# Kernel tuning notes

Hardware: AMD Instinct MI355X
Metric: run time of the kernel (lower is better)

Reference implementation:

```python
import jax, jax.numpy as jnp
import numpy as np

K_SIM_SCHEDULE = [4, 8, 16]
K_CON_SCHEDULE = [2, 4, 8]
NEG = 1000000000.0


def _dual_adjacency(h, k_sim, k_con):
    """Binary causal dual adjacency (similar / dissimilar), no gradient."""
    B, T, D = h.shape
    h = jax.lax.stop_gradient(h)
    xn = h / jnp.maximum(jnp.linalg.norm(h, axis=-1, keepdims=True), 1e-12)
    sim = jnp.einsum('btd,bsd->bts', xn, xn)                 # (B,T,T)
    past = jnp.tril(jnp.ones((T, T), h.dtype), -1)           # strictly-past mask
    sim = sim * past - NEG * (1.0 - past)
    eff_sim = min(k_sim, T - 1)
    eff_con = min(k_con, max(0, T - 1 - eff_sim))
    bI = jnp.arange(B)[:, None, None]
    tI = jnp.arange(T)[None, :, None]
    A_sim = jnp.zeros((B, T, T), h.dtype)
    if eff_sim > 0:
        _, top_idx = jax.lax.top_k(sim, eff_sim)             # (B,T,k)
        A_sim = A_sim.at[bI, tI, top_idx].set(1.0) * past
    A_con = jnp.zeros((B, T, T), h.dtype)
    if eff_con > 0:
        sim_con = jnp.where(A_sim > 0, NEG, sim)
        _, bot_idx = jax.lax.top_k(-sim_con, eff_con)        # smallest eff_con
        A_con = A_con.at[bI, tI, bot_idx].set(1.0) * past * (1.0 - A_sim)
    return A_sim, A_con


def _aggregate(h, A):
    # unweighted mean over selected neighbors; empty rows -> zeros
    deg = jnp.sum(A, axis=-1, keepdims=True)
    return jnp.einsum('bts,bsd->btd', A, h) / jnp.maximum(deg, 1.0)


def setup_inputs() -> dict:
    key = jax.random.key(0)
    ks = jax.random.split(key, 2)
    B, T, D, R = 4, 2048, 512, 3
    x = jax.random.normal(ks[0], (B, T, D), dtype=jnp.float32)
    gain = jnp.ones((R, D), dtype=jnp.float32)
    bias = jnp.zeros((R, D), dtype=jnp.float32)
    log_mix = jnp.zeros((R,), dtype=jnp.float32)
    log_alpha = jnp.zeros((R,), dtype=jnp.float32)
    log_momentum = jnp.asarray(1.0, dtype=jnp.float32)
    log_scale = jnp.asarray(0.0, dtype=jnp.float32)
    return {"x": x, "gain": gain, "bias": bias, "log_mix": log_mix,
            "log_alpha": log_alpha, "log_momentum": log_momentum,
            "log_scale": log_scale}


def reference(x, gain, bias, log_mix, log_alpha, log_momentum, log_scale):
    momentum = jax.nn.sigmoid(log_momentum)
    scale = jax.nn.softplus(log_scale) + 0.01
    h = x
    for r in range(len(K_SIM_SCHEDULE)):
        mix = jax.nn.sigmoid(log_mix[r])
        alpha = jax.nn.sigmoid(log_alpha[r])
        A_sim, A_con = _dual_adjacency(h, K_SIM_SCHEDULE[r], K_CON_SCHEDULE[r])
        msg_pos = _aggregate(h, A_sim)
        msg_neg = _aggregate(h, A_con)
        ctx = alpha * msg_pos + (1.0 - alpha) * msg_neg
        blended = mix * h + (1.0 - mix) * ctx
        h_new = jax.nn.gelu(blended * gain[r] + bias[r], approximate=False)
        h = momentum * h + (1.0 - momentum) * h_new
    return (h - x) * scale
```

## Files before the change

kernel.cpp:

```cpp
#include <hip/hip_runtime.h>
#include <hip/hip_bf16.h>
#include <cstdint>
#include <cstddef>

#define BB 4
#define TT 2048
#define DD 512
#define NEG_INF (-3.402823466e+38f)
#define POS_INF (3.402823466e+38f)

typedef __attribute__((ext_vector_type(8))) short bf16x8;
typedef __attribute__((ext_vector_type(8))) unsigned short ushort8;
typedef __attribute__((ext_vector_type(4))) float f32x4;

__device__ __forceinline__ float sigmoidf_(float x){ return 1.0f/(1.0f+expf(-x)); }

__device__ __forceinline__ unsigned short f2bf(float x){
  __hip_bfloat16 b = __float2bfloat16(x);
  return *reinterpret_cast<unsigned short*>(&b);
}

__device__ __forceinline__ unsigned int fwd_map(float f){
  unsigned int b = __float_as_uint(f);
  return b ^ ((b & 0x80000000u) ? 0xFFFFFFFFu : 0x80000000u);
}
__device__ __forceinline__ float inv_map(unsigned int u){
  unsigned int b = (u & 0x80000000u) ? (u ^ 0x80000000u) : ~u;
  return __uint_as_float(b);
}

__global__ __launch_bounds__(64) void k_normsplit(const float* __restrict__ h, float* __restrict__ rnorm,
                                                  unsigned short* __restrict__ Xh, unsigned short* __restrict__ Xl){
  int row = blockIdx.x;
  const float* hr = h + (size_t)row*DD;
  int lane = threadIdx.x;
  float4 v0 = *(const float4*)&hr[lane*4];
  float4 v1 = *(const float4*)&hr[lane*4 + 256];
  float ss = v0.x*v0.x+v0.y*v0.y+v0.z*v0.z+v0.w*v0.w
           + v1.x*v1.x+v1.y*v1.y+v1.z*v1.z+v1.w*v1.w;
  #pragma unroll
  for (int off=32; off; off>>=1) ss += __shfl_xor(ss, off);
  float rn = 1.0f / fmaxf(sqrtf(ss), 1e-12f);
  if (lane==0) rnorm[row] = rn;

  float xs[8] = {v0.x,v0.y,v0.z,v0.w,v1.x,v1.y,v1.z,v1.w};
  unsigned short hb[8], lb[8];
  #pragma unroll
  for (int q=0;q<8;q++){
    float xn = xs[q]*rn;
    unsigned short hh = f2bf(xn);
    __hip_bfloat16 bh = *reinterpret_cast<__hip_bfloat16*>(&hh);
    float rem = xn - __bfloat162float(bh);
    hb[q] = hh; lb[q] = f2bf(rem);
  }
  ushort4 h0 = {hb[0],hb[1],hb[2],hb[3]}, h1 = {hb[4],hb[5],hb[6],hb[7]};
  ushort4 l0 = {lb[0],lb[1],lb[2],lb[3]}, l1 = {lb[4],lb[5],lb[6],lb[7]};
  *(ushort4*)&Xh[(size_t)row*DD + lane*4]       = h0;
  *(ushort4*)&Xh[(size_t)row*DD + lane*4 + 256] = h1;
  *(ushort4*)&Xl[(size_t)row*DD + lane*4]       = l0;
  *(ushort4*)&Xl[(size_t)row*DD + lane*4 + 256] = l1;
}

__global__ __launch_bounds__(256) void k_sim(const unsigned short* __restrict__ Xh,
                                             const unsigned short* __restrict__ Xl,
                                             float* __restrict__ sim, int b0){
  int p = blockIdx.x;
  int jt = (int)((sqrtf(8.0f*(float)p + 1.0f) - 1.0f)*0.5f);
  while ((jt+1)*(jt+2)/2 <= p) jt++;
  while (jt*(jt+1)/2 > p) jt--;
  int is = p - jt*(jt+1)/2;

  int bl = blockIdx.y;
  size_t xoff = (size_t)(b0 + bl)*TT*DD;
  const unsigned short* XhB = Xh + xoff;
  const unsigned short* XlB = Xl + xoff;
  float* simb = sim + (size_t)bl*TT*TT;
  int t0 = jt*128, s0 = is*128;

  __shared__ __align__(16) short As[128*32];
  __shared__ __align__(16) short Bs[128*32];

  int tid = threadIdx.x, wave = tid>>6, lane = tid&63;
  int wr = wave>>1, wc = wave&1;

  int srow = tid>>2;
  int sc8  = (tid&3)*8;

  f32x4 acc[4][4];
  #pragma unroll
  for (int m=0;m<4;m++)
    #pragma unroll
    for (int n=0;n<4;n++) acc[m][n] = (f32x4){0.f,0.f,0.f,0.f};

  ushort8 ra0, ra1, rb0, rb1;
  auto gload = [&](int s){
    int pass = s>>4; int kcol = (s&15)*32;
    const unsigned short* sA = (pass<2) ? XhB : XlB;
    const unsigned short* sB = (pass!=1) ? XhB : XlB;
    ra0 = *(const ushort8*)&sA[(size_t)(t0+srow)*DD + kcol + sc8];
    ra1 = *(const ushort8*)&sA[(size_t)(t0+srow+64)*DD + kcol + sc8];
    rb0 = *(const ushort8*)&sB[(size_t)(s0+srow)*DD + kcol + sc8];
    rb1 = *(const ushort8*)&sB[(size_t)(s0+srow+64)*DD + kcol + sc8];
  };

  gload(0);
  for (int s=0; s<48; ++s){
    __syncthreads();
    *(ushort8*)&As[srow*32 + sc8]      = ra0;
    *(ushort8*)&As[(srow+64)*32 + sc8] = ra1;
    *(ushort8*)&Bs[srow*32 + sc8]      = rb0;
    *(ushort8*)&Bs[(srow+64)*32 + sc8] = rb1;
    __syncthreads();
    if (s < 47) gload(s+1);

    int arow = wr*64 + (lane&15);
    int brow = wc*64 + (lane&15);
    int kb = (lane>>4)*8;
    bf16x8 af[4], bf[4];
    #pragma unroll
    for (int m=0;m<4;m++) af[m] = *(const bf16x8*)&As[(arow + m*16)*32 + kb];
    #pragma unroll
    for (int n=0;n<4;n++) bf[n] = *(const bf16x8*)&Bs[(brow + n*16)*32 + kb];
    #pragma unroll
    for (int m=0;m<4;m++)
      #pragma unroll
      for (int n=0;n<4;n++)
        acc[m][n] = __builtin_amdgcn_mfma_f32_16x16x32_bf16(af[m], bf[n], acc[m][n], 0, 0, 0);
  }

  #pragma unroll
  for (int m=0;m<4;m++){
    int t = t0 + wr*64 + m*16 + (lane>>4)*4;
    #pragma unroll
    for (int n=0;n<4;n++){
      int sc = s0 + wc*64 + n*16 + (lane&15);
      float* dst = simb + (size_t)t*TT + sc;
      #pragma unroll
      for (int j=0;j<4;j++) dst[(size_t)j*TT] = acc[m][n][j];
    }
  }
}

template<int ESIM, int ECON>
__global__ __launch_bounds__(256) void k_topk(const float* __restrict__ sim, int b0,
                                              const float* __restrict__ h, const float* __restrict__ rnorm,
                                              int* __restrict__ topidx, int* __restrict__ botidx,
                                              int* __restrict__ bcnt){
  constexpr int K1 = ESIM + 8;
  constexpr int EQCAP = 44;
  constexpr float TAU = 5e-5f;
  __shared__ unsigned int s_u[4][TT];
  __shared__ int s_hist[4][256];
  __shared__ int s_cand[4][K1];
  __shared__ int s_eq[4][EQCAP];
  __shared__ int s_sel[4][ESIM];
  __shared__ int s_bot[4][ECON + 8];

  int tid = threadIdx.x, lane = tid & 63, wid = tid >> 6;
  int lrow = blockIdx.x*4 + wid;
  int bl = lrow >> 11, t = lrow & (TT-1);
  int gb = b0 + bl;
  int grow = (gb << 11) | t;

  if (t <= ESIM){
    if (lane < t) topidx[(size_t)grow*16 + lane] = lane;
    if (lane == 0) bcnt[grow] = 0;
    return;
  }
  const float* srow = sim + (size_t)lrow*TT;
  const float* hb  = h + (size_t)gb*TT*DD;
  const float* rnb = rnorm + (size_t)gb*TT;

  unsigned int* su = s_u[wid];
  int* sh = s_hist[wid];
  int* scand = s_cand[wid];
  int* seq   = s_eq[wid];
  int* ssel  = s_sel[wid];
  int* sbot  = s_bot[wid];

  #pragma unroll
  for (int i=0;i<4;i++) sh[lane + i*64] = 0;
  int t4 = t & ~3;
  for (int s4 = lane*4; s4 < t4; s4 += 256){
    float4 f = *(const float4*)&srow[s4];
    unsigned int u0=fwd_map(f.x), u1=fwd_map(f.y), u2=fwd_map(f.z), u3=fwd_map(f.w);
    *(uint4*)&su[s4] = (uint4){u0,u1,u2,u3};
    atomicAdd(&sh[u0>>24],1); atomicAdd(&sh[u1>>24],1);
    atomicAdd(&sh[u2>>24],1); atomicAdd(&sh[u3>>24],1);
  }
  for (int s = t4 + lane; s < t; s += 64){
    unsigned int u = fwd_map(srow[s]);
    su[s] = u; atomicAdd(&sh[u>>24],1);
  }

  unsigned int pfx = 0u; int kp = min(t, K1);
  #pragma unroll
  for (int pass = 0; pass < 4; ++pass){
    int shift = 24 - 8*pass;
    int m4 = sh[4*lane] + sh[4*lane+1] + sh[4*lane+2] + sh[4*lane+3];
    int x = __shfl(m4, 63-lane);
    #pragma unroll
    for (int off = 1; off < 64; off <<= 1){
      int v = __shfl_up(x, off);
      if (lane >= off) x += v;
    }
    int T = __shfl(x, 63-lane);
    int G = T - m4;
    bool hit = (G < kp) && (kp <= T);
    unsigned int npfx = 0u; int nkp = 0;
    if (hit){
      int c = G; int D = 4*lane;
      #pragma unroll
      for (int i = 3; i >= 0; --i){
        int hc = sh[4*lane + i];
        if (kp <= c + hc){ D = 4*lane + i; break; }
        c += hc;
      }
      npfx = pfx | ((unsigned int)D << shift);
      nkp = kp - c;
    }
    unsigned long long hm = __ballot(hit);
    int src = __ffsll(hm) - 1;
    pfx = __shfl(npfx, src);
    kp  = __shfl(nkp, src);
    if (pass == 3) break;

    int nshift = shift - 8;
    unsigned int keep = 0xFFFFFFFFu << shift;
    #pragma unroll
    for (int i=0;i<4;i++) sh[lane + i*64] = 0;
    for (int s4 = lane*4; s4 < t4; s4 += 256){
      uint4 u = *(const uint4*)&su[s4];
      if (((u.x ^ pfx) & keep) == 0) atomicAdd(&sh[(u.x>>nshift)&255],1);
      if (((u.y ^ pfx) & keep) == 0) atomicAdd(&sh[(u.y>>nshift)&255],1);
      if (((u.z ^ pfx) & keep) == 0) atomicAdd(&sh[(u.z>>nshift)&255],1);
      if (((u.w ^ pfx) & keep) == 0) atomicAdd(&sh[(u.w>>nshift)&255],1);
    }
    for (int s = t4 + lane; s < t; s += 64){
      unsigned int u = su[s];
      if (((u ^ pfx) & keep) == 0) atomicAdd(&sh[(u>>nshift)&255],1);
    }
  }
  unsigned int uthr = pfx;

  int ngt = 0, neq = 0;
  {
    unsigned long long below = (lane == 0) ? 0ull : ((~0ull) >> (64 - lane));
    for (int sb = 0; sb < t; sb += 64){
      int s = sb + lane;
      bool in = (s < t);
      unsigned int u = in ? su[s] : 0u;
      bool g = in && (u > uthr), e = in && (u == uthr);
      unsigned long long mg = __ballot(g), me = __ballot(e);
      if (g) scand[ngt + __popcll(mg & below)] = s;
      if (e){
        int pos = neq + __popcll(me & below);
        if (pos < EQCAP) seq[pos] = s;
      }
      ngt += __popcll(mg); neq += __popcll(me);
    }
  }

  int c_gt = ngt;
  int c_eq = min(neq, EQCAP);
  int ncand = min(c_gt + c_eq, 64);

  unsigned int myu = 0u; int myi = 0x7fffffff;
  if (lane < ncand){
    myi = (lane < c_gt) ? scand[lane] : seq[lane - c_gt];
    myu = su[myi];
  }

  float vA = 0.f, vB = 0.f;
  {
    unsigned int cu = myu; int ci = myi;
    #pragma unroll
    for (int k = 0; k <= ESIM; ++k){
      unsigned int bu = cu; int bi = ci;
      #pragma unroll
      for (int off=32; off; off>>=1){
        unsigned int ou = __shfl_xor(bu, off); int oi = __shfl_xor(bi, off);
        if (ou > bu || (ou == bu && oi < bi)){ bu = ou; bi = oi; }
      }
      if (k < ESIM && lane == 0) ssel[k] = bi;
      if (k == ESIM-1) vA = inv_map(bu);
      if (k == ESIM)   vB = inv_map(bu);
      if (ci == bi){ cu = 0u; ci = 0x7fffffff; }
    }
  }

  bool resc = (vA - vB < TAU);
  if (resc){
    const float* hq = hb + (size_t)t*DD;
    float rt = rnb[t];
    float4 q0 = *(const float4*)&hq[lane*4];
    float4 q1 = *(const float4*)&hq[lane*4 + 256];
    float ev = NEG_INF;
    for (int j = 0; j < ncand; ++j){
      int idx = (j < c_gt) ? scand[j] : seq[j - c_gt];
      const float* hc = hb + (size_t)idx*DD;
      float4 c0 = *(const float4*)&hc[lane*4];
      float4 c1 = *(const float4*)&hc[lane*4 + 256];
      float pp = q0.x*c0.x+q0.y*c0.y+q0.z*c0.z+q0.w*c0.w
               + q1.x*c1.x+q1.y*c1.y+q1.z*c1.z+q1.w*c1.w;
      #pragma unroll
      for (int off=32; off; off>>=1) pp += __shfl_xor(pp, off);
      float ex = pp * rt * rnb[idx];
      if (lane == j) ev = ex;
    }
    float rv = (lane < ncand) ? ev : NEG_INF;
    int   ri = myi;
    #pragma unroll
    for (int k = 0; k < ESIM; ++k){
      float bv = rv; int bi = ri;
      #pragma unroll
      for (int off=32; off; off>>=1){
        float ov = __shfl_xor(bv, off); int oi = __shfl_xor(bi, off);
        if (ov > bv || (ov == bv && oi < bi)){ bv = ov; bi = oi; }
      }
      if (lane == 0) ssel[k] = bi;
      if (ri == bi) rv = NEG_INF;
    }
  }
  if (lane < ESIM) topidx[(size_t)grow*16 + lane] = ssel[lane];

  int need = ECON - (TT - t);
  int cnt = 0;
  if (need > 0){
    if (lane < ESIM) su[ssel[lane]] = 0xFFFFFFFFu;
    int nb_ext = min(need + 8, t - ESIM);
    float wA = 0.f, wB = 0.f;
    for (int k = 0; k < nb_ext; ++k){
      unsigned int mu = 0xFFFFFFFFu; int mi = 0x7fffffff;
      for (int s = lane; s < t; s += 64){
        unsigned int u = su[s];
        if (u < mu || (u == mu && s < mi)){ mu = u; mi = s; }
      }
      #pragma unroll
      for (int off=32; off; off>>=1){
        unsigned int ou = __shfl_xor(mu, off); int oi = __shfl_xor(mi, off);
        if (ou < mu || (ou == mu && oi < mi)){ mu = ou; mi = oi; }
      }
      if (lane == 0){ sbot[k] = mi; su[mi] = 0xFFFFFFFFu; }
      if (k == need-1) wA = inv_map(mu);
      if (k == need)   wB = inv_map(mu);
    }
    cnt = need;
    bool rb = (nb_ext > need) && (wB - wA < TAU);
    if (!rb){
      if (lane < need) botidx[(size_t)grow*8 + lane] = sbot[lane];
    } else {
      const float* hq = hb + (size_t)t*DD;
      float rt = rnb[t];
      float4 q0 = *(const float4*)&hq[lane*4];
      float4 q1 = *(const float4*)&hq[lane*4 + 256];
      float ev = POS_INF; int ei = 0x7fffffff;
      for (int j = 0; j < nb_ext; ++j){
        int idx = sbot[j];
        const float* hc = hb + (size_t)idx*DD;
        float4 c0 = *(const float4*)&hc[lane*4];
        float4 c1 = *(const float4*)&hc[lane*4 + 256];
        float pp = q0.x*c0.x+q0.y*c0.y+q0.z*c0.z+q0.w*c0.w
                 + q1.x*c1.x+q1.y*c1.y+q1.z*c1.z+q1.w*c1.w;
        #pragma unroll
        for (int off=32; off; off>>=1) pp += __shfl_xor(pp, off);
        float ex = pp * rt * rnb[idx];
        if (lane == j){ ev = ex; ei = idx; }
      }
      #pragma unroll
      for (int k = 0; k < ECON; ++k){
        if (k < need){
          float bv = ev; int bi = ei;
          #pragma unroll
          for (int off=32; off; off>>=1){
            float ov = __shfl_xor(bv, off); int oi = __shfl_xor(bi, off);
            if (ov < bv || (ov == bv && oi < bi)){ bv = ov; bi = oi; }
          }
          if (lane == 0) botidx[(size_t)grow*8 + k] = bi;
          if (ei == bi) ev = POS_INF;
        }
      }
    }
  }
  if (lane == 0) bcnt[grow] = cnt;
}

__global__ __launch_bounds__(256) void k_agg(const float* __restrict__ hsrc, float* __restrict__ hdst,
                                             const int* __restrict__ topidx, const int* __restrict__ botidx,
                                             const int* __restrict__ bcnt,
                                             const float* __restrict__ gain, const float* __restrict__ bias,
                                             const float* __restrict__ log_mix, const float* __restrict__ log_alpha,
                                             const float* __restrict__ log_momentum, int r, int eff_sim){
  int row = blockIdx.x;
  int b = row >> 11; int t = row & (TT-1);
  int n_sim = min(eff_sim, t);
  int n_con = bcnt[row];
  float mix      = sigmoidf_(log_mix[r]);
  float alpha    = sigmoidf_(log_alpha[r]);
  float momentum = sigmoidf_(log_momentum[0]);
  const float* hb = hsrc + (size_t)b*TT*DD;

  __shared__ int sidx[16];
  __shared__ int scidx[8];
  if (threadIdx.x < 16) sidx[threadIdx.x]  = (threadIdx.x < n_sim) ? topidx[(size_t)row*16 + threadIdx.x] : 0;
  if (threadIdx.x < 8)  scidx[threadIdx.x] = (threadIdx.x < n_con) ? botidx[(size_t)row*8  + threadIdx.x] : 0;
  __syncthreads();

  #pragma unroll
  for (int e = threadIdx.x; e < DD; e += 256){
    float sp = 0.f;
    for (int j=0;j<n_sim;j++) sp += hb[(size_t)sidx[j]*DD + e];
    float sn = 0.f;
    for (int j=0;j<n_con;j++) sn += hb[(size_t)scidx[j]*DD + e];
    float mp = sp / (float)max(n_sim, 1);
    float mn = sn / (float)max(n_con, 1);
    float ctx = alpha*mp + (1.f-alpha)*mn;
    float hv = hsrc[(size_t)row*DD + e];
    float blended = mix*hv + (1.f-mix)*ctx;
    float u = blended*gain[e] + bias[e];
    float g = 0.5f*u*(1.0f + erff(u*0.7071067811865475f));
    hdst[(size_t)row*DD + e] = momentum*hv + (1.f-momentum)*g;
  }
}

__global__ __launch_bounds__(256) void k_final(const float* __restrict__ hfin, const float* __restrict__ x,
                                               const float* __restrict__ log_scale, float* __restrict__ out, int n){
  float scale = log1pf(expf(log_scale[0])) + 0.01f;
  int i = blockIdx.x*256 + threadIdx.x;
  if (i < n) out[i] = (hfin[i] - x[i]) * scale;
}

extern "C" void kernel_launch(void* const* d_in, const int* in_sizes, int n_in,
                              void* d_out, int out_size, void* d_ws, size_t ws_size,
                              hipStream_t stream) {
  const float* x         = (const float*)d_in[0];
  const float* gain      = (const float*)d_in[1];
  const float* bias      = (const float*)d_in[2];
  const float* log_mix   = (const float*)d_in[3];
  const float* log_alpha = (const float*)d_in[4];
  const float* log_mom   = (const float*)d_in[5];
  const float* log_scale = (const float*)d_in[6];

  float* hA = (float*)d_out;
  char* ws = (char*)d_ws;
  size_t off = 0;
  auto alloc = [&](size_t bytes){ void* p = ws + off; off += (bytes + 255) & ~(size_t)255; return p; };

  float*          hB     = (float*)alloc((size_t)BB*TT*DD*4);
  float*          rnorm  = (float*)alloc((size_t)BB*TT*4);
  int*            topidx = (int*)  alloc((size_t)BB*TT*16*4);
  int*            botidx = (int*)  alloc((size_t)BB*TT*8*4);
  int*            bcnt   = (int*)  alloc((size_t)BB*TT*4);
  unsigned short* Xh     = (unsigned short*)alloc((size_t)BB*TT*DD*2);
  unsigned short* Xl     = (unsigned short*)alloc((size_t)BB*TT*DD*2);

  size_t rem = (ws_size > off) ? (ws_size - off) : 0;
  int cb = (int)(rem / ((size_t)TT*TT*4));
  if (cb < 1) cb = 1;
  if (cb > BB) cb = BB;
  float* sim = (float*)alloc((size_t)cb*TT*TT*4);

  const float* hsrc = x;
  float* hdst = hB;
  const int ks[3] = {4, 8, 16};

  for (int r = 0; r < 3; ++r){
    k_normsplit<<<BB*TT, 64, 0, stream>>>(hsrc, rnorm, Xh, Xl);
    for (int b0 = 0; b0 < BB; b0 += cb){
      int nb = (BB - b0 < cb) ? (BB - b0) : cb;
      dim3 g(136, nb);
      k_sim<<<g, 256, 0, stream>>>(Xh, Xl, sim, b0);
      if (r == 0)      k_topk<4,2><<<nb*TT/4, 256, 0, stream>>>(sim, b0, hsrc, rnorm, topidx, botidx, bcnt);
      else if (r == 1) k_topk<8,4><<<nb*TT/4, 256, 0, stream>>>(sim, b0, hsrc, rnorm, topidx, botidx, bcnt);
      else             k_topk<16,8><<<nb*TT/4, 256, 0, stream>>>(sim, b0, hsrc, rnorm, topidx, botidx, bcnt);
    }
    k_agg<<<BB*TT, 256, 0, stream>>>(hsrc, hdst, topidx, botidx, bcnt,
                                     gain + (size_t)r*DD, bias + (size_t)r*DD,
                                     log_mix, log_alpha, log_mom, r, ks[r]);
    if (r == 0){ hsrc = hB; hdst = hA; }
    else if (r == 1){ hsrc = hA; hdst = hB; }
  }
  k_final<<<(BB*TT*DD)/256, 256, 0, stream>>>(hB, x, log_scale, (float*)d_out, BB*TT*DD);
}
```

Measured before the change: 552.2 us.

## Drop per-row LDS staging in top-k; use 24-bit radix select for bottom-k

The top-k kernel no longer stages each row's mapped keys in a 32 KB shared buffer. Instead it re-reads the similarity row from global or L2 on each radix pass, cuts the radix to three 8-bit passes, and collects candidates with shared atomics. The bottom-k path swaps its repeated full-row argmin scans for a second radix select on flipped keys plus a wave-level selection that skips indices already chosen as top-k. This frees most of the LDS to raise occupancy and removes the O(k·t) bottom scan, at the cost of more global reads and candidate lists that can overflow their fixed caps.

```diff
diff --git a/kernel.cpp b/kernel.cpp
--- a/kernel.cpp
+++ b/kernel.cpp
@@ -141,61 +141,26 @@
   }
 }
 
-template<int ESIM, int ECON>
-__global__ __launch_bounds__(256) void k_topk(const float* __restrict__ sim, int b0,
-                                              const float* __restrict__ h, const float* __restrict__ rnorm,
-                                              int* __restrict__ topidx, int* __restrict__ botidx,
-                                              int* __restrict__ bcnt){
-  constexpr int K1 = ESIM + 8;
-  constexpr int EQCAP = 44;
-  constexpr float TAU = 5e-5f;
-  __shared__ unsigned int s_u[4][TT];
-  __shared__ int s_hist[4][256];
-  __shared__ int s_cand[4][K1];
-  __shared__ int s_eq[4][EQCAP];
-  __shared__ int s_sel[4][ESIM];
-  __shared__ int s_bot[4][ECON + 8];
-
-  int tid = threadIdx.x, lane = tid & 63, wid = tid >> 6;
-  int lrow = blockIdx.x*4 + wid;
-  int bl = lrow >> 11, t = lrow & (TT-1);
-  int gb = b0 + bl;
-  int grow = (gb << 11) | t;
-
-  if (t <= ESIM){
-    if (lane < t) topidx[(size_t)grow*16 + lane] = lane;
-    if (lane == 0) bcnt[grow] = 0;
-    return;
-  }
-  const float* srow = sim + (size_t)lrow*TT;
-  const float* hb  = h + (size_t)gb*TT*DD;
-  const float* rnb = rnorm + (size_t)gb*TT;
-
-  unsigned int* su = s_u[wid];
-  int* sh = s_hist[wid];
-  int* scand = s_cand[wid];
-  int* seq   = s_eq[wid];
-  int* ssel  = s_sel[wid];
-  int* sbot  = s_bot[wid];
-
+#define BMASK 0xFFFFFF00u
+
+__device__ __forceinline__ unsigned int radix24(const float* __restrict__ srow, int t, int k1,
+                                                unsigned int flip, int* sh, int lane){
   #pragma unroll
   for (int i=0;i<4;i++) sh[lane + i*64] = 0;
   int t4 = t & ~3;
   for (int s4 = lane*4; s4 < t4; s4 += 256){
     float4 f = *(const float4*)&srow[s4];
-    unsigned int u0=fwd_map(f.x), u1=fwd_map(f.y), u2=fwd_map(f.z), u3=fwd_map(f.w);
-    *(uint4*)&su[s4] = (uint4){u0,u1,u2,u3};
+    unsigned int u0=fwd_map(f.x)^flip, u1=fwd_map(f.y)^flip, u2=fwd_map(f.z)^flip, u3=fwd_map(f.w)^flip;
     atomicAdd(&sh[u0>>24],1); atomicAdd(&sh[u1>>24],1);
     atomicAdd(&sh[u2>>24],1); atomicAdd(&sh[u3>>24],1);
   }
   for (int s = t4 + lane; s < t; s += 64){
-    unsigned int u = fwd_map(srow[s]);
-    su[s] = u; atomicAdd(&sh[u>>24],1);
-  }
-
-  unsigned int pfx = 0u; int kp = min(t, K1);
-  #pragma unroll
-  for (int pass = 0; pass < 4; ++pass){
+    unsigned int u = fwd_map(srow[s])^flip;
+    atomicAdd(&sh[u>>24],1);
+  }
+  unsigned int pfx = 0u; int kp = k1;
+  #pragma unroll
+  for (int pass = 0; pass < 3; ++pass){
     int shift = 24 - 8*pass;
     int m4 = sh[4*lane] + sh[4*lane+1] + sh[4*lane+2] + sh[4*lane+3];
     int x = __shfl(m4, 63-lane);
@@ -223,52 +188,94 @@
     int src = __ffsll(hm) - 1;
     pfx = __shfl(npfx, src);
     kp  = __shfl(nkp, src);
-    if (pass == 3) break;
+    if (pass == 2) break;
 
     int nshift = shift - 8;
     unsigned int keep = 0xFFFFFFFFu << shift;
     #pragma unroll
     for (int i=0;i<4;i++) sh[lane + i*64] = 0;
     for (int s4 = lane*4; s4 < t4; s4 += 256){
-      uint4 u = *(const uint4*)&su[s4];
-      if (((u.x ^ pfx) & keep) == 0) atomicAdd(&sh[(u.x>>nshift)&255],1);
-      if (((u.y ^ pfx) & keep) == 0) atomicAdd(&sh[(u.y>>nshift)&255],1);
-      if (((u.z ^ pfx) & keep) == 0) atomicAdd(&sh[(u.z>>nshift)&255],1);
-      if (((u.w ^ pfx) & keep) == 0) atomicAdd(&sh[(u.w>>nshift)&255],1);
+      float4 f = *(const float4*)&srow[s4];
+      unsigned int u0=fwd_map(f.x)^flip, u1=fwd_map(f.y)^flip, u2=fwd_map(f.z)^flip, u3=fwd_map(f.w)^flip;
+      if (((u0 ^ pfx) & keep) == 0) atomicAdd(&sh[(u0>>nshift)&255],1);
+      if (((u1 ^ pfx) & keep) == 0) atomicAdd(&sh[(u1>>nshift)&255],1);
+      if (((u2 ^ pfx) & keep) == 0) atomicAdd(&sh[(u2>>nshift)&255],1);
+      if (((u3 ^ pfx) & keep) == 0) atomicAdd(&sh[(u3>>nshift)&255],1);
     }
     for (int s = t4 + lane; s < t; s += 64){
-      unsigned int u = su[s];
+      unsigned int u = fwd_map(srow[s])^flip;
       if (((u ^ pfx) & keep) == 0) atomicAdd(&sh[(u>>nshift)&255],1);
     }
   }
-  unsigned int uthr = pfx;
-
-  int ngt = 0, neq = 0;
-  {
-    unsigned long long below = (lane == 0) ? 0ull : ((~0ull) >> (64 - lane));
-    for (int sb = 0; sb < t; sb += 64){
-      int s = sb + lane;
-      bool in = (s < t);
-      unsigned int u = in ? su[s] : 0u;
-      bool g = in && (u > uthr), e = in && (u == uthr);
-      unsigned long long mg = __ballot(g), me = __ballot(e);
-      if (g) scand[ngt + __popcll(mg & below)] = s;
-      if (e){
-        int pos = neq + __popcll(me & below);
-        if (pos < EQCAP) seq[pos] = s;
-      }
-      ngt += __popcll(mg); neq += __popcll(me);
-    }
-  }
-
-  int c_gt = ngt;
-  int c_eq = min(neq, EQCAP);
+  return pfx;
+}
+
+template<int ESIM, int ECON>
+__global__ __launch_bounds__(256) void k_topk(const float* __restrict__ sim, int b0,
+                                              const float* __restrict__ h, const float* __restrict__ rnorm,
+                                              int* __restrict__ topidx, int* __restrict__ botidx,
+                                              int* __restrict__ bcnt){
+  constexpr int K1  = ESIM + 8;
+  constexpr int K1B = ESIM + ECON + 8;
+  constexpr int CANDCAP = 40;
+  constexpr int EQCAP = 44;
+  constexpr float TAU = 5e-5f;
+  __shared__ int s_hist[4][256];
+  __shared__ int s_cand[4][CANDCAP];
+  __shared__ int s_eq[4][EQCAP];
+  __shared__ int s_sel[4][ESIM];
+  __shared__ int s_bot[4][16];
+  __shared__ int s_cnt[4][2];
+
+  int tid = threadIdx.x, lane = tid & 63, wid = tid >> 6;
+  int lrow = blockIdx.x*4 + wid;
+  int bl = lrow >> 11, t = lrow & (TT-1);
+  int gb = b0 + bl;
+  int grow = (gb << 11) | t;
+
+  if (t <= ESIM){
+    if (lane < t) topidx[(size_t)grow*16 + lane] = lane;
+    if (lane == 0) bcnt[grow] = 0;
+    return;
+  }
+  const float* srow = sim + (size_t)lrow*TT;
+  const float* hb  = h + (size_t)gb*TT*DD;
+  const float* rnb = rnorm + (size_t)gb*TT;
+
+  int* sh    = s_hist[wid];
+  int* scand = s_cand[wid];
+  int* seq   = s_eq[wid];
+  int* ssel  = s_sel[wid];
+  int* sbot  = s_bot[wid];
+
+  int k1 = min(t, K1);
+  unsigned int thr = radix24(srow, t, k1, 0u, sh, lane);
+
+  if (lane == 0){ s_cnt[wid][0] = 0; s_cnt[wid][1] = 0; }
+  int t4 = t & ~3;
+  for (int s4 = lane*4; s4 < t4; s4 += 256){
+    float4 f = *(const float4*)&srow[s4];
+    unsigned int uu[4] = {fwd_map(f.x), fwd_map(f.y), fwd_map(f.z), fwd_map(f.w)};
+    #pragma unroll
+    for (int q=0;q<4;q++){
+      unsigned int b24 = uu[q] & BMASK;
+      if (b24 > thr){ int p = atomicAdd(&s_cnt[wid][0],1); if (p < CANDCAP) scand[p] = s4+q; }
+      else if (b24 == thr){ int p = atomicAdd(&s_cnt[wid][1],1); if (p < EQCAP) seq[p] = s4+q; }
+    }
+  }
+  for (int s = t4 + lane; s < t; s += 64){
+    unsigned int b24 = fwd_map(srow[s]) & BMASK;
+    if (b24 > thr){ int p = atomicAdd(&s_cnt[wid][0],1); if (p < CANDCAP) scand[p] = s; }
+    else if (b24 == thr){ int p = atomicAdd(&s_cnt[wid][1],1); if (p < EQCAP) seq[p] = s; }
+  }
+  int c_gt = min(s_cnt[wid][0], CANDCAP);
+  int c_eq = min(s_cnt[wid][1], EQCAP);
   int ncand = min(c_gt + c_eq, 64);
 
   unsigned int myu = 0u; int myi = 0x7fffffff;
   if (lane < ncand){
     myi = (lane < c_gt) ? scand[lane] : seq[lane - c_gt];
-    myu = su[myi];
+    myu = fwd_map(srow[myi]);
   }
 
   float vA = 0.f, vB = 0.f;
@@ -327,35 +334,71 @@
   int need = ECON - (TT - t);
   int cnt = 0;
   if (need > 0){
-    if (lane < ESIM) su[ssel[lane]] = 0xFFFFFFFFu;
-    int nb_ext = min(need + 8, t - ESIM);
+    constexpr unsigned int FLIP = 0xFFFFFFFFu;
+    int k1b = min(t, K1B);
+    unsigned int thrb = radix24(srow, t, k1b, FLIP, sh, lane);
+
+    if (lane == 0){ s_cnt[wid][0] = 0; s_cnt[wid][1] = 0; }
+    for (int s4 = lane*4; s4 < t4; s4 += 256){
+      float4 f = *(const float4*)&srow[s4];
+      unsigned int uu[4] = {fwd_map(f.x)^FLIP, fwd_map(f.y)^FLIP, fwd_map(f.z)^FLIP, fwd_map(f.w)^FLIP};
+      #pragma unroll
+      for (int q=0;q<4;q++){
+        unsigned int b24 = uu[q] & BMASK;
+        if (b24 > thrb){ int p = atomicAdd(&s_cnt[wid][0],1); if (p < CANDCAP) scand[p] = s4+q; }
+        else if (b24 == thrb){ int p = atomicAdd(&s_cnt[wid][1],1); if (p < EQCAP) seq[p] = s4+q; }
+      }
+    }
+    for (int s = t4 + lane; s < t; s += 64){
+      unsigned int u = fwd_map(srow[s])^FLIP;
+      unsigned int b24 = u & BMASK;
+      if (b24 > thrb){ int p = atomicAdd(&s_cnt[wid][0],1); if (p < CANDCAP) scand[p] = s; }
+      else if (b24 == thrb){ int p = atomicAdd(&s_cnt[wid][1],1); if (p < EQCAP) seq[p] = s; }
+    }
+    int bc_gt = min(s_cnt[wid][0], CANDCAP);
+    int bc_eq = min(s_cnt[wid][1], EQCAP);
+    int ncb = min(bc_gt + bc_eq, 64);
+
+    unsigned int mu = 0u; int mi = 0x7fffffff;
+    if (lane < ncb){
+      mi = (lane < bc_gt) ? scand[lane] : seq[lane - bc_gt];
+      mu = fwd_map(srow[mi]) ^ FLIP;
+    }
     float wA = 0.f, wB = 0.f;
-    for (int k = 0; k < nb_ext; ++k){
-      unsigned int mu = 0xFFFFFFFFu; int mi = 0x7fffffff;
-      for (int s = lane; s < t; s += 64){
-        unsigned int u = su[s];
-        if (u < mu || (u == mu && s < mi)){ mu = u; mi = s; }
-      }
-      #pragma unroll
-      for (int off=32; off; off>>=1){
-        unsigned int ou = __shfl_xor(mu, off); int oi = __shfl_xor(mi, off);
-        if (ou < mu || (ou == mu && oi < mi)){ mu = ou; mi = oi; }
-      }
-      if (lane == 0){ sbot[k] = mi; su[mi] = 0xFFFFFFFFu; }
-      if (k == need-1) wA = inv_map(mu);
-      if (k == need)   wB = inv_map(mu);
-    }
-    cnt = need;
-    bool rb = (nb_ext > need) && (wB - wA < TAU);
+    unsigned int cu = mu; int ci = mi;
+    #pragma unroll
+    for (int k = 0; k < K1B; ++k){
+      if (k < ncb && cnt < need + 8){
+        unsigned int bu = cu; int bi = ci;
+        #pragma unroll
+        for (int off=32; off; off>>=1){
+          unsigned int ou = __shfl_xor(bu, off); int oi = __shfl_xor(bi, off);
+          if (ou > bu || (ou == bu && oi < bi)){ bu = ou; bi = oi; }
+        }
+        if (ci == bi){ cu = 0u; ci = 0x7fffffff; }
+        bool mem = false;
+        #pragma unroll
+        for (int j=0;j<ESIM;j++) if (ssel[j] == bi) mem = true;
+        if (!mem){
+          if (lane == 0) sbot[cnt] = bi;
+          float val = inv_map(bu ^ FLIP);
+          if (cnt == need-1) wA = val;
+          if (cnt == need)   wB = val;
+          cnt++;
+        }
+      }
+    }
+    int npick = min(need, cnt);
+    bool rb = (cnt > need) && (wB - wA < TAU);
     if (!rb){
-      if (lane < need) botidx[(size_t)grow*8 + lane] = sbot[lane];
+      if (lane < npick) botidx[(size_t)grow*8 + lane] = sbot[lane];
     } else {
       const float* hq = hb + (size_t)t*DD;
       float rt = rnb[t];
       float4 q0 = *(const float4*)&hq[lane*4];
       float4 q1 = *(const float4*)&hq[lane*4 + 256];
       float ev = POS_INF; int ei = 0x7fffffff;
-      for (int j = 0; j < nb_ext; ++j){
+      for (int j = 0; j < cnt; ++j){
         int idx = sbot[j];
         const float* hc = hb + (size_t)idx*DD;
         float4 c0 = *(const float4*)&hc[lane*4];
@@ -369,7 +412,7 @@
       }
       #pragma unroll
       for (int k = 0; k < ECON; ++k){
-        if (k < need){
+        if (k < npick){
           float bv = ev; int bi = ei;
           #pragma unroll
           for (int off=32; off; off>>=1){
@@ -381,6 +424,7 @@
         }
       }
     }
+    cnt = npick;
   }
   if (lane == 0) bcnt[grow] = cnt;
 }
```

Measured after the change: 472.4 us. 14.4% less time.
